# Optimization experiments

Measured on AMD Instinct MI355X. Metric: run time of the kernel, lower is better.

Reference implementation:

```python
import jax, jax.numpy as jnp
import numpy as np

B, N, S, K = 8, 4096, 2048, 64          # clouds, points/cloud, fps samples (ratio=0.5), max neighbors
C_IN, HID, OUT = 64, 128, 128
RADIUS = 0.2
EPS = 1e-5


def fps(p, s):
    """Farthest point sampling on p:[N,3]; deterministic start at index 0. Returns [s] indices."""
    def step(carry, _):
        min_d, last = carry
        d = jnp.sum((p - p[last]) ** 2, axis=-1)
        min_d = jnp.minimum(min_d, d)
        return (min_d, jnp.argmax(min_d).astype(jnp.int32)), last
    init = (jnp.full((p.shape[0],), jnp.inf, p.dtype), jnp.int32(0))
    _, idx = jax.lax.scan(step, init, None, length=s)
    return idx


def bn_act(h, g, be, mask):
    # masked batch-norm over all valid edges (training-mode stats), then ReLU
    m = mask[..., None].astype(h.dtype)
    cnt = jnp.sum(m)
    mean = jnp.sum(h * m, axis=(0, 1, 2)) / cnt
    var = jnp.sum(((h - mean) ** 2) * m, axis=(0, 1, 2)) / cnt
    return jax.nn.relu((h - mean) * jax.lax.rsqrt(var + EPS) * g + be)


def setup_inputs() -> dict:
    key = jax.random.key(0)
    ks = jax.random.split(key, 8)
    x = jax.random.normal(ks[0], (B * N, C_IN), jnp.float32)
    pos = jax.random.uniform(ks[1], (B * N, 3), jnp.float32)
    batch = jnp.repeat(jnp.arange(B, dtype=jnp.int32), N)
    c0 = C_IN + 3
    W0 = jax.random.normal(ks[2], (c0, HID), jnp.float32) / np.sqrt(c0).astype(np.float32)
    W1 = jax.random.normal(ks[3], (HID, HID), jnp.float32) / np.sqrt(HID).astype(np.float32)
    W2 = jax.random.normal(ks[4], (HID, OUT), jnp.float32) / np.sqrt(HID).astype(np.float32)
    z = lambda n: jnp.zeros((n,), jnp.float32)
    o = lambda n: jnp.ones((n,), jnp.float32)
    return dict(x=x, pos=pos, batch=batch,
                W0=W0, b0=z(HID), g0=o(HID), be0=z(HID),
                W1=W1, b1=z(HID), g1=o(HID), be1=z(HID),
                W2=W2, b2=z(OUT))


def reference(x, pos, batch, W0, b0, g0, be0, W1, b1, g1, be1, W2, b2):
    posb = pos.reshape(B, N, 3)
    xb = x.reshape(B, N, C_IN)
    idx = jax.vmap(lambda p: fps(p, S))(posb)                       # [B,S]
    ctr = jnp.take_along_axis(posb, idx[..., None], axis=1)          # [B,S,3] sampled centroids
    # radius graph: K nearest within RADIUS (mask the rest)
    d2 = jnp.sum((ctr[:, :, None, :] - posb[:, None, :, :]) ** 2, axis=-1)  # [B,S,N]
    negd, nbr = jax.lax.top_k(-d2, K)                                # [B,S,K]
    mask = (-negd) <= RADIUS ** 2
    bix = jnp.arange(B)[:, None, None]
    pos_j = posb[bix, nbr]                                           # [B,S,K,3]
    x_j = xb[bix, nbr]                                               # [B,S,K,C_IN]
    feat = jnp.concatenate([x_j, pos_j - ctr[:, :, None, :]], axis=-1)  # [B,S,K,C_IN+3]
    h = bn_act(feat @ W0 + b0, g0, be0, mask)
    h = bn_act(h @ W1 + b1, g1, be1, mask)
    h = h @ W2 + b2                                                  # plain last layer
    h = jnp.where(mask[..., None], h, -jnp.inf)
    out = jnp.max(h, axis=2)                                         # max aggregation -> [B,S,OUT]
    batch_out = jnp.take_along_axis(batch.reshape(B, N), idx, axis=1).reshape(-1)
    return out.reshape(B * S, OUT), ctr.reshape(B * S, 3), batch_out
```

## Files before the change

### kernel.cpp

```cpp
#include <hip/hip_runtime.h>

typedef _Float16 half8 __attribute__((ext_vector_type(8)));
typedef float floatx4 __attribute__((ext_vector_type(4)));

#define B_   8
#define N_   4096
#define S_   2048
#define K_   64
#define CIN  64
#define HID_ 128
#define Q_   (B_*S_)
#define NCONS 248

#define WS_STATS 0u
#define WS_CNTT  4096u
#define WS_W0T   4224u
#define WS_W1T   28800u
#define WS_W2T   61568u
#define WS_SC0   94336u
#define WS_SH0   94848u
#define WS_SC1   95360u
#define WS_SH1   95872u
#define WS_CNT   96384u
#define WS_NBR   161920u
#define WS_PROG  2259072u

__global__ __launch_bounds__(256) void k_prep(const float* __restrict__ W0,
        const float* __restrict__ W1, const float* __restrict__ W2,
        _Float16* __restrict__ w0t, _Float16* __restrict__ w1t, _Float16* __restrict__ w2t,
        unsigned long long* __restrict__ stats, int* __restrict__ cntT, int* __restrict__ prog) {
    int t = blockIdx.x * 256 + threadIdx.x;
    if (t < 128 * 96) {
        int c = t / 96, k = t - c * 96;
        w0t[t] = (k < 67) ? (_Float16)W0[k * 128 + c] : (_Float16)0.f;
    } else if (t < 128 * 96 + 16384) {
        int u = t - 128 * 96; int c = u >> 7, k = u & 127;
        w1t[u] = (_Float16)W1[k * 128 + c];
    } else if (t < 128 * 96 + 32768) {
        int u = t - 128 * 96 - 16384; int c = u >> 7, k = u & 127;
        w2t[u] = (_Float16)W2[k * 128 + c];
    }
    if (t < 512) stats[t] = 0ULL;
    if (t < 8) prog[t] = 0;
    if (t == 0) *cntT = 0;
}

template<int CTRL>
__device__ inline unsigned long long dpp64(unsigned long long v) {
    int lo = (int)(unsigned)v, hi = (int)(unsigned)(v >> 32);
    int nlo = __builtin_amdgcn_update_dpp(lo, lo, CTRL, 0xF, 0xF, false);
    int nhi = __builtin_amdgcn_update_dpp(hi, hi, CTRL, 0xF, 0xF, false);
    return ((unsigned long long)(unsigned)nhi << 32) | (unsigned long long)(unsigned)nlo;
}
__device__ inline unsigned long long u64max(unsigned long long a, unsigned long long b) {
    return (b > a) ? b : a;
}

__global__ __launch_bounds__(256) void k_front(const float* __restrict__ pos,
        const float* __restrict__ x, const _Float16* __restrict__ w0t,
        const float* __restrict__ b0, float* outCtr, float* __restrict__ outBatch,
        unsigned short* __restrict__ nbrG, int* __restrict__ cnt, int* __restrict__ cntT,
        unsigned long long* __restrict__ statsOut, int* prog) {
    __shared__ __align__(16) char uLDS[69760];
    int tid = threadIdx.x;

    if (blockIdx.x < 8) {
        float4* sP4 = (float4*)uLDS;
        unsigned long long* red = (unsigned long long*)(uLDS + 65536);
        unsigned short* sSeq = (unsigned short*)(uLDS + 65600);
        int b = blockIdx.x;
        const float* P = pos + (size_t)b * N_ * 3;

        float px[16], py[16], pz[16], md[16];
        {
            const float4* vp = (const float4*)(P + tid * 48);
            float a[48];
            #pragma unroll
            for (int v = 0; v < 12; v++) {
                float4 t4 = vp[v];
                a[v*4] = t4.x; a[v*4+1] = t4.y; a[v*4+2] = t4.z; a[v*4+3] = t4.w;
            }
            #pragma unroll
            for (int j = 0; j < 16; j++) {
                px[j] = a[3*j]; py[j] = a[3*j+1]; pz[j] = a[3*j+2];
                md[j] = __builtin_inff();
                sP4[tid * 16 + j] = make_float4(px[j], py[j], pz[j], 0.f);
            }
        }
        __syncthreads();

        int last = 0;
        for (int i = 0; i < S_; i++) {
            float4 cc = sP4[last];
            if (tid == (i & 255)) sSeq[i] = (unsigned short)last;
            unsigned long long best;
            {
                #pragma clang fp contract(off)
                float bv = -1.f; unsigned bi = 0;
                #pragma unroll
                for (int j = 0; j < 16; j++) {
                    float dx = px[j] - cc.x, dy = py[j] - cc.y, dz = pz[j] - cc.z;
                    float d = (dx * dx + dy * dy) + dz * dz;
                    float m = fminf(md[j], d); md[j] = m;
                    if (m > bv) { bv = m; bi = (unsigned)j; }
                }
                best = ((unsigned long long)__float_as_uint(bv) << 32)
                     | (unsigned long long)(0xFFFFu - (unsigned)(tid * 16) - bi);
            }
            best = u64max(best, dpp64<0x111>(best));
            best = u64max(best, dpp64<0x112>(best));
            best = u64max(best, dpp64<0x114>(best));
            best = u64max(best, dpp64<0x118>(best));
            best = u64max(best, dpp64<0x142>(best));
            best = u64max(best, dpp64<0x143>(best));
            if ((tid & 63) == 63) red[(i & 1) * 4 + (tid >> 6)] = best;
            __syncthreads();
            ulonglong2 ra = *(const ulonglong2*)&red[(i & 1) * 4];
            ulonglong2 rb = *(const ulonglong2*)&red[(i & 1) * 4 + 2];
            unsigned long long g = u64max(u64max(ra.x, ra.y), u64max(rb.x, rb.y));
            last = (int)(0xFFFFu - (unsigned)(g & 0xFFFFu));
            if ((i & 63) == 63) {
                if (tid < 64) {
                    int ii = i - 63 + tid;
                    float4 c = sP4[sSeq[ii]];
                    size_t o = (size_t)b * S_ + ii;
                    __hip_atomic_store(&outCtr[o*3],   c.x, __ATOMIC_RELAXED, __HIP_MEMORY_SCOPE_AGENT);
                    __hip_atomic_store(&outCtr[o*3+1], c.y, __ATOMIC_RELAXED, __HIP_MEMORY_SCOPE_AGENT);
                    __hip_atomic_store(&outCtr[o*3+2], c.z, __ATOMIC_RELAXED, __HIP_MEMORY_SCOPE_AGENT);
                    outBatch[o] = (float)b;
                }
                __syncthreads();
                if (tid == 0)
                    __hip_atomic_store(&prog[b], i + 1, __ATOMIC_RELEASE, __HIP_MEMORY_SCOPE_AGENT);
            }
        }
    } else {
        float* cD = (float*)uLDS;
        unsigned short* cI = (unsigned short*)(uLDS + 4096);
        unsigned short* sNbr = (unsigned short*)(uLDS + 6144);
        float* sB0v = (float*)(uLDS + 6272);
        float* sCtr = (float*)(uLDS + 6784);
        int* cN = (int*)(uLDS + 6800);
        _Float16* sBuf = (_Float16*)(uLDS + 6912);

        int wid = tid >> 6, lane = tid & 63;
        int lr = lane & 15, lq = lane >> 4;
        int colbase = 32 * wid + lr;
        half8 w0f[3][2];
        #pragma unroll
        for (int ks = 0; ks < 3; ks++)
            #pragma unroll
            for (int nt = 0; nt < 2; nt++)
                w0f[ks][nt] = *(const half8*)(w0t + (colbase + 16*nt) * 96 + ks * 32 + lq * 8);
        if (tid < 128) sB0v[tid] = b0[tid];
        float runS1[2] = {0.f, 0.f}, runS2[2] = {0.f, 0.f};

        for (int k = (int)blockIdx.x - 8; k < Q_; k += NCONS) {
            int i = k >> 3, b = k & 7;
            int q = (b << 11) + i;
            if (tid == 0) {
                while (__hip_atomic_load(&prog[b], __ATOMIC_ACQUIRE, __HIP_MEMORY_SCOPE_AGENT) <= i)
                    __builtin_amdgcn_s_sleep(32);
                sCtr[0] = __hip_atomic_load(&outCtr[(size_t)q*3],   __ATOMIC_RELAXED, __HIP_MEMORY_SCOPE_AGENT);
                sCtr[1] = __hip_atomic_load(&outCtr[(size_t)q*3+1], __ATOMIC_RELAXED, __HIP_MEMORY_SCOPE_AGENT);
                sCtr[2] = __hip_atomic_load(&outCtr[(size_t)q*3+2], __ATOMIC_RELAXED, __HIP_MEMORY_SCOPE_AGENT);
                *cN = 0;
            }
            __syncthreads();
            float cx = sCtr[0], cy = sCtr[1], cz = sCtr[2];
            const float* P = pos + (size_t)b * N_ * 3;
            float a[48];
            {
                const float4* vp = (const float4*)(P + (size_t)tid * 48);
                #pragma unroll
                for (int v = 0; v < 12; v++) {
                    float4 t4 = vp[v];
                    a[v*4] = t4.x; a[v*4+1] = t4.y; a[v*4+2] = t4.z; a[v*4+3] = t4.w;
                }
            }
            unsigned msk = 0;
            float d2a[16];
            {
                #pragma clang fp contract(off)
                #pragma unroll
                for (int j = 0; j < 16; j++) {
                    float dx = cx - a[3*j], dy = cy - a[3*j+1], dz = cz - a[3*j+2];
                    float d2 = (dx * dx + dy * dy) + dz * dz;
                    d2a[j] = d2;
                    if (d2 <= 0.04f) msk |= 1u << j;
                }
            }
            int myc = __popc(msk);
            int base = 0;
            if (myc) base = atomicAdd(cN, myc);
            unsigned mm = msk;
            while (mm) {
                int j = __builtin_ctz(mm); mm &= mm - 1;
                if (base < 1024) { cD[base] = d2a[j]; cI[base] = (unsigned short)(tid * 16 + j); }
                base++;
            }
            __syncthreads();
            int M = min(*cN, 1024);
            int n = min(M, K_);
            for (int i2 = tid; i2 < M; i2 += 256) {
                float di = cD[i2]; int ii = (int)cI[i2]; int r = 0;
                for (int j = 0; j < M; j++) {
                    float dj = cD[j];
                    r += (dj < di) || (dj == di && (int)cI[j] < ii);
                }
                if (r < K_) { nbrG[q * K_ + r] = (unsigned short)ii; sNbr[r] = (unsigned short)ii; }
            }
            if (tid == 0) { cnt[q] = n; atomicAdd(cntT, n); }
            __syncthreads();
            {
                int row = tid >> 2, c4 = (tid & 3) * 16;
                half8 o0, o1;
                #pragma unroll
                for (int e = 0; e < 8; e++) { o0[e] = (_Float16)0.f; o1[e] = (_Float16)0.f; }
                if (row < n) {
                    const float4* xr = (const float4*)(x + ((size_t)b * N_ + sNbr[row]) * CIN + c4);
                    float4 v0 = xr[0], v1 = xr[1], v2 = xr[2], v3 = xr[3];
                    o0[0]=(_Float16)v0.x; o0[1]=(_Float16)v0.y; o0[2]=(_Float16)v0.z; o0[3]=(_Float16)v0.w;
                    o0[4]=(_Float16)v1.x; o0[5]=(_Float16)v1.y; o0[6]=(_Float16)v1.z; o0[7]=(_Float16)v1.w;
                    o1[0]=(_Float16)v2.x; o1[1]=(_Float16)v2.y; o1[2]=(_Float16)v2.z; o1[3]=(_Float16)v2.w;
                    o1[4]=(_Float16)v3.x; o1[5]=(_Float16)v3.y; o1[6]=(_Float16)v3.z; o1[7]=(_Float16)v3.w;
                }
                *(half8*)&sBuf[row * 104 + c4]     = o0;
                *(half8*)&sBuf[row * 104 + c4 + 8] = o1;
            }
            if (tid < 64) {
                half8 z, o;
                #pragma unroll
                for (int e = 0; e < 8; e++) { z[e] = (_Float16)0.f; o[e] = (_Float16)0.f; }
                if (tid < n) {
                    int j = sNbr[tid];
                    const float* pj = pos + ((size_t)b * N_ + j) * 3;
                    o[0] = (_Float16)(pj[0] - cx); o[1] = (_Float16)(pj[1] - cy); o[2] = (_Float16)(pj[2] - cz);
                }
                *(half8*)&sBuf[tid * 104 + 64] = o;
                *(half8*)&sBuf[tid * 104 + 72] = z;
                *(half8*)&sBuf[tid * 104 + 80] = z;
                *(half8*)&sBuf[tid * 104 + 88] = z;
            }
            __syncthreads();
            floatx4 acc[4][2];
            #pragma unroll
            for (int rt = 0; rt < 4; rt++)
                #pragma unroll
                for (int nt = 0; nt < 2; nt++)
                    #pragma unroll
                    for (int r = 0; r < 4; r++) acc[rt][nt][r] = 0.f;
            #pragma unroll
            for (int ks = 0; ks < 3; ks++) {
                half8 av[4];
                #pragma unroll
                for (int rt = 0; rt < 4; rt++)
                    av[rt] = *(const half8*)&sBuf[(rt * 16 + lr) * 104 + ks * 32 + lq * 8];
                #pragma unroll
                for (int rt = 0; rt < 4; rt++)
                    #pragma unroll
                    for (int nt = 0; nt < 2; nt++)
                        acc[rt][nt] = __builtin_amdgcn_mfma_f32_16x16x32_f16(av[rt], w0f[ks][nt], acc[rt][nt], 0, 0, 0);
            }
            #pragma unroll
            for (int nt = 0; nt < 2; nt++) {
                int col = colbase + 16 * nt;
                float bias = sB0v[col];
                #pragma unroll
                for (int rt = 0; rt < 4; rt++) {
                    int r0 = rt * 16 + lq * 4;
                    #pragma unroll
                    for (int r = 0; r < 4; r++) {
                        float v = acc[rt][nt][r] + bias;
                        if (r0 + r < n) { runS1[nt] += v; runS2[nt] += v * v; }
                    }
                }
            }
        }
        #pragma unroll
        for (int nt = 0; nt < 2; nt++) {
            float s1 = runS1[nt], s2 = runS2[nt];
            s1 += __shfl_xor(s1, 16); s1 += __shfl_xor(s1, 32);
            s2 += __shfl_xor(s2, 16); s2 += __shfl_xor(s2, 32);
            if (lq == 0) {
                int col = colbase + 16 * nt;
                atomicAdd(&statsOut[col],       (unsigned long long)(long long)llrintf(s1 * 1048576.f));
                atomicAdd(&statsOut[128 + col], (unsigned long long)(long long)llrintf(s2 * 1048576.f));
            }
        }
    }
}

__global__ void k_bnparam(const unsigned long long* __restrict__ stats, const int* __restrict__ cntT,
        const float* __restrict__ g, const float* __restrict__ be,
        float* __restrict__ scale, float* __restrict__ shift) {
    int t = threadIdx.x;
    double c = (double)(*cntT);
    double mean = (double)(long long)stats[t] * (1.0 / 1048576.0) / c;
    double ex2  = (double)(long long)stats[128 + t] * (1.0 / 1048576.0) / c;
    double var = ex2 - mean * mean;
    if (var < 0.0) var = 0.0;
    double sc = (double)g[t] / sqrt(var + 1e-5);
    scale[t] = (float)sc;
    shift[t] = (float)((double)be[t] - mean * sc);
}

template<int STAGE>
__global__ __launch_bounds__(256, 2) void k_mlp(const float* __restrict__ x,
        const float* __restrict__ pos, const float* __restrict__ ctr,
        const unsigned short* __restrict__ nbr, const int* __restrict__ cnt,
        const _Float16* __restrict__ w0t, const _Float16* __restrict__ w1t,
        const _Float16* __restrict__ w2t,
        const float* __restrict__ b0, const float* __restrict__ b1,
        const float* __restrict__ b2,
        const float* __restrict__ sc0, const float* __restrict__ sh0,
        const float* __restrict__ sc1, const float* __restrict__ sh1,
        unsigned long long* __restrict__ statsOut, float* __restrict__ outF) {
    __shared__ __align__(16) _Float16 sBuf[64 * 136];
    __shared__ unsigned short sNbr[64];
    __shared__ float sB0v[128];
    __shared__ float sB1v[128];
    __shared__ float sSc0[128];
    __shared__ float sSh0[128];
    __shared__ float sB2v[(STAGE >= 2) ? 128 : 4];
    __shared__ float sSc1[(STAGE >= 2) ? 128 : 4];
    __shared__ float sSh1[(STAGE >= 2) ? 128 : 4];

    int tid = threadIdx.x, wid = tid >> 6, lane = tid & 63;
    int lr = lane & 15, lq = lane >> 4;
    int colbase = 32 * wid + lr;

    half8 w0f[3][2];
    #pragma unroll
    for (int ks = 0; ks < 3; ks++)
        #pragma unroll
        for (int nt = 0; nt < 2; nt++)
            w0f[ks][nt] = *(const half8*)(w0t + (colbase + 16*nt) * 96 + ks * 32 + lq * 8);
    half8 w1f[4][2];
    #pragma unroll
    for (int ks = 0; ks < 4; ks++)
        #pragma unroll
        for (int nt = 0; nt < 2; nt++)
            w1f[ks][nt] = *(const half8*)(w1t + (colbase + 16*nt) * 128 + ks * 32 + lq * 8);
    half8 w2f[(STAGE >= 2) ? 4 : 1][2];
    if constexpr (STAGE >= 2)
        #pragma unroll
        for (int ks = 0; ks < 4; ks++)
            #pragma unroll
            for (int nt = 0; nt < 2; nt++)
                w2f[ks][nt] = *(const half8*)(w2t + (colbase + 16*nt) * 128 + ks * 32 + lq * 8);

    if (tid < 128) {
        sB0v[tid] = b0[tid];
        sB1v[tid] = b1[tid]; sSc0[tid] = sc0[tid]; sSh0[tid] = sh0[tid];
        if constexpr (STAGE >= 2) { sB2v[tid] = b2[tid]; sSc1[tid] = sc1[tid]; sSh1[tid] = sh1[tid]; }
    }
    float runS1[2] = {0.f, 0.f}, runS2[2] = {0.f, 0.f};

    for (int qq = 0; qq < 8; qq++) {
        int q = blockIdx.x * 8 + qq;
        int b = q >> 11;
        __syncthreads();
        int n = cnt[q];
        if (tid < 64) sNbr[tid] = nbr[q * K_ + tid];
        __syncthreads();
        {
            int row = tid >> 2, c4 = (tid & 3) * 16;
            half8 o0, o1;
            #pragma unroll
            for (int e = 0; e < 8; e++) { o0[e] = (_Float16)0.f; o1[e] = (_Float16)0.f; }
            if (row < n) {
                const float4* xr = (const float4*)(x + ((size_t)b * N_ + sNbr[row]) * CIN + c4);
                float4 v0 = xr[0], v1 = xr[1], v2 = xr[2], v3 = xr[3];
                o0[0]=(_Float16)v0.x; o0[1]=(_Float16)v0.y; o0[2]=(_Float16)v0.z; o0[3]=(_Float16)v0.w;
                o0[4]=(_Float16)v1.x; o0[5]=(_Float16)v1.y; o0[6]=(_Float16)v1.z; o0[7]=(_Float16)v1.w;
                o1[0]=(_Float16)v2.x; o1[1]=(_Float16)v2.y; o1[2]=(_Float16)v2.z; o1[3]=(_Float16)v2.w;
                o1[4]=(_Float16)v3.x; o1[5]=(_Float16)v3.y; o1[6]=(_Float16)v3.z; o1[7]=(_Float16)v3.w;
            }
            *(half8*)&sBuf[row * 104 + c4]     = o0;
            *(half8*)&sBuf[row * 104 + c4 + 8] = o1;
        }
        if (tid < 64) {
            half8 z, o;
            #pragma unroll
            for (int e = 0; e < 8; e++) { z[e] = (_Float16)0.f; o[e] = (_Float16)0.f; }
            if (tid < n) {
                int j = sNbr[tid];
                float cx = ctr[q*3], cy = ctr[q*3+1], cz = ctr[q*3+2];
                const float* pj = pos + ((size_t)b * N_ + j) * 3;
                o[0] = (_Float16)(pj[0] - cx); o[1] = (_Float16)(pj[1] - cy); o[2] = (_Float16)(pj[2] - cz);
            }
            *(half8*)&sBuf[tid * 104 + 64] = o;
            *(half8*)&sBuf[tid * 104 + 72] = z;
            *(half8*)&sBuf[tid * 104 + 80] = z;
            *(half8*)&sBuf[tid * 104 + 88] = z;
        }
        __syncthreads();

        floatx4 acc[4][2];
        #pragma unroll
        for (int rt = 0; rt < 4; rt++)
            #pragma unroll
            for (int nt = 0; nt < 2; nt++)
                #pragma unroll
                for (int r = 0; r < 4; r++) acc[rt][nt][r] = 0.f;
        #pragma unroll
        for (int ks = 0; ks < 3; ks++) {
            half8 av[4];
            #pragma unroll
            for (int rt = 0; rt < 4; rt++)
                av[rt] = *(const half8*)&sBuf[(rt * 16 + lr) * 104 + ks * 32 + lq * 8];
            #pragma unroll
            for (int rt = 0; rt < 4; rt++)
                #pragma unroll
                for (int nt = 0; nt < 2; nt++)
                    acc[rt][nt] = __builtin_amdgcn_mfma_f32_16x16x32_f16(av[rt], w0f[ks][nt], acc[rt][nt], 0, 0, 0);
        }
        __syncthreads();

        #pragma unroll
        for (int nt = 0; nt < 2; nt++) {
            int col = colbase + 16 * nt;
            float bias = sB0v[col], s = sSc0[col], t2 = sSh0[col];
            #pragma unroll
            for (int rt = 0; rt < 4; rt++) {
                int r0 = rt * 16 + lq * 4;
                #pragma unroll
                for (int r = 0; r < 4; r++) {
                    float v = (acc[rt][nt][r] + bias) * s + t2;
                    sBuf[(r0 + r) * 136 + col] = (_Float16)fmaxf(v, 0.f);
                }
            }
        }
        __syncthreads();
        #pragma unroll
        for (int rt = 0; rt < 4; rt++)
            #pragma unroll
            for (int nt = 0; nt < 2; nt++)
                #pragma unroll
                for (int r = 0; r < 4; r++) acc[rt][nt][r] = 0.f;
        #pragma unroll
        for (int ks = 0; ks < 4; ks++) {
            half8 av[4];
            #pragma unroll
            for (int rt = 0; rt < 4; rt++)
                av[rt] = *(const half8*)&sBuf[(rt * 16 + lr) * 136 + ks * 32 + lq * 8];
            #pragma unroll
            for (int rt = 0; rt < 4; rt++)
                #pragma unroll
                for (int nt = 0; nt < 2; nt++)
                    acc[rt][nt] = __builtin_amdgcn_mfma_f32_16x16x32_f16(av[rt], w1f[ks][nt], acc[rt][nt], 0, 0, 0);
        }

        if constexpr (STAGE == 1) {
            #pragma unroll
            for (int nt = 0; nt < 2; nt++) {
                int col = colbase + 16 * nt;
                float bias = sB1v[col];
                #pragma unroll
                for (int rt = 0; rt < 4; rt++) {
                    int r0 = rt * 16 + lq * 4;
                    #pragma unroll
                    for (int r = 0; r < 4; r++) {
                        float v = acc[rt][nt][r] + bias;
                        if (r0 + r < n) { runS1[nt] += v; runS2[nt] += v * v; }
                    }
                }
            }
        } else {
            __syncthreads();
            #pragma unroll
            for (int nt = 0; nt < 2; nt++) {
                int col = colbase + 16 * nt;
                float bias = sB1v[col], s = sSc1[col], t2 = sSh1[col];
                #pragma unroll
                for (int rt = 0; rt < 4; rt++) {
                    int r0 = rt * 16 + lq * 4;
                    #pragma unroll
                    for (int r = 0; r < 4; r++) {
                        float v = (acc[rt][nt][r] + bias) * s + t2;
                        sBuf[(r0 + r) * 136 + col] = (_Float16)fmaxf(v, 0.f);
                    }
                }
            }
            __syncthreads();
            #pragma unroll
            for (int rt = 0; rt < 4; rt++)
                #pragma unroll
                for (int nt = 0; nt < 2; nt++)
                    #pragma unroll
                    for (int r = 0; r < 4; r++) acc[rt][nt][r] = 0.f;
            #pragma unroll
            for (int ks = 0; ks < 4; ks++) {
                half8 av[4];
                #pragma unroll
                for (int rt = 0; rt < 4; rt++)
                    av[rt] = *(const half8*)&sBuf[(rt * 16 + lr) * 136 + ks * 32 + lq * 8];
                #pragma unroll
                for (int rt = 0; rt < 4; rt++)
                    #pragma unroll
                    for (int nt = 0; nt < 2; nt++)
                        acc[rt][nt] = __builtin_amdgcn_mfma_f32_16x16x32_f16(av[rt], w2f[ks][nt], acc[rt][nt], 0, 0, 0);
            }
            #pragma unroll
            for (int nt = 0; nt < 2; nt++) {
                int col = colbase + 16 * nt;
                float bias = sB2v[col];
                float m = -__builtin_inff();
                #pragma unroll
                for (int rt = 0; rt < 4; rt++) {
                    int r0 = rt * 16 + lq * 4;
                    #pragma unroll
                    for (int r = 0; r < 4; r++)
                        if (r0 + r < n) m = fmaxf(m, acc[rt][nt][r] + bias);
                }
                m = fmaxf(m, __shfl_xor(m, 16));
                m = fmaxf(m, __shfl_xor(m, 32));
                if (lq == 0) outF[(size_t)q * 128 + col] = m;
            }
        }
    }
    if constexpr (STAGE == 1) {
        #pragma unroll
        for (int nt = 0; nt < 2; nt++) {
            float s1 = runS1[nt], s2 = runS2[nt];
            s1 += __shfl_xor(s1, 16); s1 += __shfl_xor(s1, 32);
            s2 += __shfl_xor(s2, 16); s2 += __shfl_xor(s2, 32);
            if (lq == 0) {
                int col = colbase + 16 * nt;
                atomicAdd(&statsOut[col],       (unsigned long long)(long long)llrintf(s1 * 1048576.f));
                atomicAdd(&statsOut[128 + col], (unsigned long long)(long long)llrintf(s2 * 1048576.f));
            }
        }
    }
}

extern "C" void kernel_launch(void* const* d_in, const int* in_sizes, int n_in,
                              void* d_out, int out_size, void* d_ws, size_t ws_size,
                              hipStream_t stream) {
    const float* x   = (const float*)d_in[0];
    const float* pos = (const float*)d_in[1];
    const float* W0  = (const float*)d_in[3];
    const float* b0  = (const float*)d_in[4];
    const float* g0  = (const float*)d_in[5];
    const float* be0 = (const float*)d_in[6];
    const float* W1  = (const float*)d_in[7];
    const float* b1  = (const float*)d_in[8];
    const float* g1  = (const float*)d_in[9];
    const float* be1 = (const float*)d_in[10];
    const float* W2  = (const float*)d_in[11];
    const float* b2  = (const float*)d_in[12];

    char* ws = (char*)d_ws;
    unsigned long long* stats = (unsigned long long*)(ws + WS_STATS);
    int* cntT = (int*)(ws + WS_CNTT);
    _Float16* w0t = (_Float16*)(ws + WS_W0T);
    _Float16* w1t = (_Float16*)(ws + WS_W1T);
    _Float16* w2t = (_Float16*)(ws + WS_W2T);
    float* sc0 = (float*)(ws + WS_SC0);
    float* sh0 = (float*)(ws + WS_SH0);
    float* sc1 = (float*)(ws + WS_SC1);
    float* sh1 = (float*)(ws + WS_SH1);
    int* cnt = (int*)(ws + WS_CNT);
    unsigned short* nbr = (unsigned short*)(ws + WS_NBR);
    int* prog = (int*)(ws + WS_PROG);

    float* outF = (float*)d_out;
    float* outCtr = (float*)d_out + 2097152;
    float* outBatch = (float*)d_out + 2146304;

    k_prep<<<176, 256, 0, stream>>>(W0, W1, W2, w0t, w1t, w2t, stats, cntT, prog);
    k_front<<<256, 256, 0, stream>>>(pos, x, w0t, b0, outCtr, outBatch, nbr, cnt, cntT,
            stats, prog);
    k_bnparam<<<1, 128, 0, stream>>>(stats, cntT, g0, be0, sc0, sh0);
    k_mlp<1><<<Q_/8, 256, 0, stream>>>(x, pos, outCtr, nbr, cnt, w0t, w1t, w2t,
            b0, b1, b2, sc0, sh0, sc1, sh1, stats + 256, outF);
    k_bnparam<<<1, 128, 0, stream>>>(stats + 256, cntT, g1, be1, sc1, sh1);
    k_mlp<2><<<Q_/8, 256, 0, stream>>>(x, pos, outCtr, nbr, cnt, w0t, w1t, w2t,
            b0, b1, b2, sc0, sh0, sc1, sh1, stats, outF);
}
```

Baseline: 1.743 ms.

## Materialize first-layer pre-activations in workspace to skip recomputation in MLP stages

```diff
diff --git a/kernel.cpp b/kernel.cpp
--- a/kernel.cpp
+++ b/kernel.cpp
@@ -24,6 +24,8 @@
 #define WS_CNT   96384u
 #define WS_NBR   161920u
 #define WS_PROG  2259072u
+#define WS_H0    2260992u
+#define H0_BYTES 268435456ULL
 
 __global__ __launch_bounds__(256) void k_prep(const float* __restrict__ W0,
         const float* __restrict__ W1, const float* __restrict__ W2,
@@ -60,8 +62,9 @@
         const float* __restrict__ x, const _Float16* __restrict__ w0t,
         const float* __restrict__ b0, float* outCtr, float* __restrict__ outBatch,
         unsigned short* __restrict__ nbrG, int* __restrict__ cnt, int* __restrict__ cntT,
-        unsigned long long* __restrict__ statsOut, int* prog) {
-    __shared__ __align__(16) char uLDS[69760];
+        unsigned long long* __restrict__ statsOut, int* prog,
+        _Float16* __restrict__ h0, int doH0) {
+    __shared__ __align__(16) char uLDS[84480];
     int tid = threadIdx.x;
 
     if (blockIdx.x < 8) {
@@ -142,6 +145,7 @@
         float* sCtr = (float*)(uLDS + 6784);
         int* cN = (int*)(uLDS + 6800);
         _Float16* sBuf = (_Float16*)(uLDS + 6912);
+        _Float16* sOut = (_Float16*)(uLDS + 20224);
 
         int wid = tid >> 6, lane = tid & 63;
         int lr = lane & 15, lq = lane >> 4;
@@ -273,8 +277,15 @@
                     for (int r = 0; r < 4; r++) {
                         float v = acc[rt][nt][r] + bias;
                         if (r0 + r < n) { runS1[nt] += v; runS2[nt] += v * v; }
+                        if (doH0) sOut[(r0 + r) * 128 + col] = (_Float16)v;
                     }
                 }
+            }
+            if (doH0) {
+                __syncthreads();
+                const float4* src = (const float4*)sOut;
+                float4* dst = (float4*)(h0 + (size_t)q * 8192);
+                for (int i2 = tid; i2 < 1024; i2 += 256) dst[i2] = src[i2];
             }
         }
         #pragma unroll
@@ -305,7 +316,7 @@
     shift[t] = (float)((double)be[t] - mean * sc);
 }
 
-template<int STAGE>
+template<int STAGE, int BIG>
 __global__ __launch_bounds__(256, 2) void k_mlp(const float* __restrict__ x,
         const float* __restrict__ pos, const float* __restrict__ ctr,
         const unsigned short* __restrict__ nbr, const int* __restrict__ cnt,
@@ -315,7 +326,8 @@
         const float* __restrict__ b2,
         const float* __restrict__ sc0, const float* __restrict__ sh0,
         const float* __restrict__ sc1, const float* __restrict__ sh1,
-        unsigned long long* __restrict__ statsOut, float* __restrict__ outF) {
+        unsigned long long* __restrict__ statsOut, const _Float16* __restrict__ h0,
+        float* __restrict__ outF) {
     __shared__ __align__(16) _Float16 sBuf[64 * 136];
     __shared__ unsigned short sNbr[64];
     __shared__ float sB0v[128];
@@ -330,12 +342,13 @@
     int lr = lane & 15, lq = lane >> 4;
     int colbase = 32 * wid + lr;
 
-    half8 w0f[3][2];
-    #pragma unroll
-    for (int ks = 0; ks < 3; ks++)
-        #pragma unroll
-        for (int nt = 0; nt < 2; nt++)
-            w0f[ks][nt] = *(const half8*)(w0t + (colbase + 16*nt) * 96 + ks * 32 + lq * 8);
+    half8 w0f[BIG ? 1 : 3][2];
+    if constexpr (!BIG)
+        #pragma unroll
+        for (int ks = 0; ks < 3; ks++)
+            #pragma unroll
+            for (int nt = 0; nt < 2; nt++)
+                w0f[ks][nt] = *(const half8*)(w0t + (colbase + 16*nt) * 96 + ks * 32 + lq * 8);
     half8 w1f[4][2];
     #pragma unroll
     for (int ks = 0; ks < 4; ks++)
@@ -362,77 +375,95 @@
         int b = q >> 11;
         __syncthreads();
         int n = cnt[q];
-        if (tid < 64) sNbr[tid] = nbr[q * K_ + tid];
-        __syncthreads();
-        {
-            int row = tid >> 2, c4 = (tid & 3) * 16;
-            half8 o0, o1;
-            #pragma unroll
-            for (int e = 0; e < 8; e++) { o0[e] = (_Float16)0.f; o1[e] = (_Float16)0.f; }
-            if (row < n) {
-                const float4* xr = (const float4*)(x + ((size_t)b * N_ + sNbr[row]) * CIN + c4);
-                float4 v0 = xr[0], v1 = xr[1], v2 = xr[2], v3 = xr[3];
-                o0[0]=(_Float16)v0.x; o0[1]=(_Float16)v0.y; o0[2]=(_Float16)v0.z; o0[3]=(_Float16)v0.w;
-                o0[4]=(_Float16)v1.x; o0[5]=(_Float16)v1.y; o0[6]=(_Float16)v1.z; o0[7]=(_Float16)v1.w;
-                o1[0]=(_Float16)v2.x; o1[1]=(_Float16)v2.y; o1[2]=(_Float16)v2.z; o1[3]=(_Float16)v2.w;
-                o1[4]=(_Float16)v3.x; o1[5]=(_Float16)v3.y; o1[6]=(_Float16)v3.z; o1[7]=(_Float16)v3.w;
-            }
-            *(half8*)&sBuf[row * 104 + c4]     = o0;
-            *(half8*)&sBuf[row * 104 + c4 + 8] = o1;
-        }
-        if (tid < 64) {
-            half8 z, o;
-            #pragma unroll
-            for (int e = 0; e < 8; e++) { z[e] = (_Float16)0.f; o[e] = (_Float16)0.f; }
-            if (tid < n) {
-                int j = sNbr[tid];
-                float cx = ctr[q*3], cy = ctr[q*3+1], cz = ctr[q*3+2];
-                const float* pj = pos + ((size_t)b * N_ + j) * 3;
-                o[0] = (_Float16)(pj[0] - cx); o[1] = (_Float16)(pj[1] - cy); o[2] = (_Float16)(pj[2] - cz);
-            }
-            *(half8*)&sBuf[tid * 104 + 64] = o;
-            *(half8*)&sBuf[tid * 104 + 72] = z;
-            *(half8*)&sBuf[tid * 104 + 80] = z;
-            *(half8*)&sBuf[tid * 104 + 88] = z;
-        }
-        __syncthreads();
-
         floatx4 acc[4][2];
-        #pragma unroll
-        for (int rt = 0; rt < 4; rt++)
-            #pragma unroll
-            for (int nt = 0; nt < 2; nt++)
-                #pragma unroll
-                for (int r = 0; r < 4; r++) acc[rt][nt][r] = 0.f;
-        #pragma unroll
-        for (int ks = 0; ks < 3; ks++) {
-            half8 av[4];
+
+        if constexpr (BIG) {
+            int row = tid >> 2, c0 = (tid & 3) * 32;
+            const _Float16* hp = h0 + (size_t)q * 8192 + row * 128 + c0;
+            #pragma unroll
+            for (int g2 = 0; g2 < 4; g2++) {
+                half8 hv = *(const half8*)(hp + g2 * 8);
+                half8 ov;
+                #pragma unroll
+                for (int e = 0; e < 8; e++) {
+                    int c = c0 + g2 * 8 + e;
+                    float v = (float)hv[e] * sSc0[c] + sSh0[c];
+                    ov[e] = (_Float16)fmaxf(v, 0.f);
+                }
+                *(half8*)&sBuf[row * 136 + c0 + g2 * 8] = ov;
+            }
+            __syncthreads();
+        } else {
+            if (tid < 64) sNbr[tid] = nbr[q * K_ + tid];
+            __syncthreads();
+            {
+                int row = tid >> 2, c4 = (tid & 3) * 16;
+                half8 o0, o1;
+                #pragma unroll
+                for (int e = 0; e < 8; e++) { o0[e] = (_Float16)0.f; o1[e] = (_Float16)0.f; }
+                if (row < n) {
+                    const float4* xr = (const float4*)(x + ((size_t)b * N_ + sNbr[row]) * CIN + c4);
+                    float4 v0 = xr[0], v1 = xr[1], v2 = xr[2], v3 = xr[3];
+                    o0[0]=(_Float16)v0.x; o0[1]=(_Float16)v0.y; o0[2]=(_Float16)v0.z; o0[3]=(_Float16)v0.w;
+                    o0[4]=(_Float16)v1.x; o0[5]=(_Float16)v1.y; o0[6]=(_Float16)v1.z; o0[7]=(_Float16)v1.w;
+                    o1[0]=(_Float16)v2.x; o1[1]=(_Float16)v2.y; o1[2]=(_Float16)v2.z; o1[3]=(_Float16)v2.w;
+                    o1[4]=(_Float16)v3.x; o1[5]=(_Float16)v3.y; o1[6]=(_Float16)v3.z; o1[7]=(_Float16)v3.w;
+                }
+                *(half8*)&sBuf[row * 104 + c4]     = o0;
+                *(half8*)&sBuf[row * 104 + c4 + 8] = o1;
+            }
+            if (tid < 64) {
+                half8 z, o;
+                #pragma unroll
+                for (int e = 0; e < 8; e++) { z[e] = (_Float16)0.f; o[e] = (_Float16)0.f; }
+                if (tid < n) {
+                    int j = sNbr[tid];
+                    float cx = ctr[q*3], cy = ctr[q*3+1], cz = ctr[q*3+2];
+                    const float* pj = pos + ((size_t)b * N_ + j) * 3;
+                    o[0] = (_Float16)(pj[0] - cx); o[1] = (_Float16)(pj[1] - cy); o[2] = (_Float16)(pj[2] - cz);
+                }
+                *(half8*)&sBuf[tid * 104 + 64] = o;
+                *(half8*)&sBuf[tid * 104 + 72] = z;
+                *(half8*)&sBuf[tid * 104 + 80] = z;
+                *(half8*)&sBuf[tid * 104 + 88] = z;
+            }
+            __syncthreads();
             #pragma unroll
             for (int rt = 0; rt < 4; rt++)
-                av[rt] = *(const half8*)&sBuf[(rt * 16 + lr) * 104 + ks * 32 + lq * 8];
-            #pragma unroll
-            for (int rt = 0; rt < 4; rt++)
                 #pragma unroll
                 for (int nt = 0; nt < 2; nt++)
-                    acc[rt][nt] = __builtin_amdgcn_mfma_f32_16x16x32_f16(av[rt], w0f[ks][nt], acc[rt][nt], 0, 0, 0);
-        }
-        __syncthreads();
-
-        #pragma unroll
-        for (int nt = 0; nt < 2; nt++) {
-            int col = colbase + 16 * nt;
-            float bias = sB0v[col], s = sSc0[col], t2 = sSh0[col];
-            #pragma unroll
-            for (int rt = 0; rt < 4; rt++) {
-                int r0 = rt * 16 + lq * 4;
-                #pragma unroll
-                for (int r = 0; r < 4; r++) {
-                    float v = (acc[rt][nt][r] + bias) * s + t2;
-                    sBuf[(r0 + r) * 136 + col] = (_Float16)fmaxf(v, 0.f);
-                }
-            }
-        }
-        __syncthreads();
+                    #pragma unroll
+                    for (int r = 0; r < 4; r++) acc[rt][nt][r] = 0.f;
+            #pragma unroll
+            for (int ks = 0; ks < 3; ks++) {
+                half8 av[4];
+                #pragma unroll
+                for (int rt = 0; rt < 4; rt++)
+                    av[rt] = *(const half8*)&sBuf[(rt * 16 + lr) * 104 + ks * 32 + lq * 8];
+                #pragma unroll
+                for (int rt = 0; rt < 4; rt++)
+                    #pragma unroll
+                    for (int nt = 0; nt < 2; nt++)
+                        acc[rt][nt] = __builtin_amdgcn_mfma_f32_16x16x32_f16(av[rt], w0f[ks][nt], acc[rt][nt], 0, 0, 0);
+            }
+            __syncthreads();
+            #pragma unroll
+            for (int nt = 0; nt < 2; nt++) {
+                int col = colbase + 16 * nt;
+                float bias = sB0v[col], s = sSc0[col], t2 = sSh0[col];
+                #pragma unroll
+                for (int rt = 0; rt < 4; rt++) {
+                    int r0 = rt * 16 + lq * 4;
+                    #pragma unroll
+                    for (int r = 0; r < 4; r++) {
+                        float v = (acc[rt][nt][r] + bias) * s + t2;
+                        sBuf[(r0 + r) * 136 + col] = (_Float16)fmaxf(v, 0.f);
+                    }
+                }
+            }
+            __syncthreads();
+        }
+
         #pragma unroll
         for (int rt = 0; rt < 4; rt++)
             #pragma unroll
@@ -564,6 +595,8 @@
     int* cnt = (int*)(ws + WS_CNT);
     unsigned short* nbr = (unsigned short*)(ws + WS_NBR);
     int* prog = (int*)(ws + WS_PROG);
+    _Float16* h0 = (_Float16*)(ws + WS_H0);
+    int big = (ws_size >= (size_t)WS_H0 + H0_BYTES) ? 1 : 0;
 
     float* outF = (float*)d_out;
     float* outCtr = (float*)d_out + 2097152;
@@ -571,11 +604,19 @@
 
     k_prep<<<176, 256, 0, stream>>>(W0, W1, W2, w0t, w1t, w2t, stats, cntT, prog);
     k_front<<<256, 256, 0, stream>>>(pos, x, w0t, b0, outCtr, outBatch, nbr, cnt, cntT,
-            stats, prog);
+            stats, prog, h0, big);
     k_bnparam<<<1, 128, 0, stream>>>(stats, cntT, g0, be0, sc0, sh0);
-    k_mlp<1><<<Q_/8, 256, 0, stream>>>(x, pos, outCtr, nbr, cnt, w0t, w1t, w2t,
-            b0, b1, b2, sc0, sh0, sc1, sh1, stats + 256, outF);
-    k_bnparam<<<1, 128, 0, stream>>>(stats + 256, cntT, g1, be1, sc1, sh1);
-    k_mlp<2><<<Q_/8, 256, 0, stream>>>(x, pos, outCtr, nbr, cnt, w0t, w1t, w2t,
-            b0, b1, b2, sc0, sh0, sc1, sh1, stats, outF);
+    if (big) {
+        k_mlp<1,1><<<Q_/8, 256, 0, stream>>>(x, pos, outCtr, nbr, cnt, w0t, w1t, w2t,
+                b0, b1, b2, sc0, sh0, sc1, sh1, stats + 256, h0, outF);
+        k_bnparam<<<1, 128, 0, stream>>>(stats + 256, cntT, g1, be1, sc1, sh1);
+        k_mlp<2,1><<<Q_/8, 256, 0, stream>>>(x, pos, outCtr, nbr, cnt, w0t, w1t, w2t,
+                b0, b1, b2, sc0, sh0, sc1, sh1, stats, h0, outF);
+    } else {
+        k_mlp<1,0><<<Q_/8, 256, 0, stream>>>(x, pos, outCtr, nbr, cnt, w0t, w1t, w2t,
+                b0, b1, b2, sc0, sh0, sc1, sh1, stats + 256, h0, outF);
+        k_bnparam<<<1, 128, 0, stream>>>(stats + 256, cntT, g1, be1, sc1, sh1);
+        k_mlp<2,0><<<Q_/8, 256, 0, stream>>>(x, pos, outCtr, nbr, cnt, w0t, w1t, w2t,
+                b0, b1, b2, sc0, sh0, sc1, sh1, stats, h0, outF);
+    }
 }
```

Result: no change. 1.749 ms (+0.4%).

## Fold BN param kernels into MLP, publish FPS indices instead of centroids

Applied to the files above, without the earlier changes.

```diff
diff --git a/kernel.cpp b/kernel.cpp
--- a/kernel.cpp
+++ b/kernel.cpp
@@ -17,13 +17,10 @@
 #define WS_W0T   4224u
 #define WS_W1T   28800u
 #define WS_W2T   61568u
-#define WS_SC0   94336u
-#define WS_SH0   94848u
-#define WS_SC1   95360u
-#define WS_SH1   95872u
 #define WS_CNT   96384u
 #define WS_NBR   161920u
 #define WS_PROG  2259072u
+#define WS_IDX   2259200u
 
 __global__ __launch_bounds__(256) void k_prep(const float* __restrict__ W0,
         const float* __restrict__ W1, const float* __restrict__ W2,
@@ -58,10 +55,10 @@
 
 __global__ __launch_bounds__(256) void k_front(const float* __restrict__ pos,
         const float* __restrict__ x, const _Float16* __restrict__ w0t,
-        const float* __restrict__ b0, float* outCtr, float* __restrict__ outBatch,
+        const float* __restrict__ b0, float* __restrict__ outCtr, float* __restrict__ outBatch,
         unsigned short* __restrict__ nbrG, int* __restrict__ cnt, int* __restrict__ cntT,
-        unsigned long long* __restrict__ statsOut, int* prog) {
-    __shared__ __align__(16) char uLDS[69760];
+        unsigned long long* __restrict__ statsOut, int* prog, int* idxG) {
+    __shared__ __align__(16) char uLDS[84480];
     int tid = threadIdx.x;
 
     if (blockIdx.x < 8) {
@@ -122,17 +119,20 @@
             if ((i & 63) == 63) {
                 if (tid < 64) {
                     int ii = i - 63 + tid;
-                    float4 c = sP4[sSeq[ii]];
-                    size_t o = (size_t)b * S_ + ii;
-                    __hip_atomic_store(&outCtr[o*3],   c.x, __ATOMIC_RELAXED, __HIP_MEMORY_SCOPE_AGENT);
-                    __hip_atomic_store(&outCtr[o*3+1], c.y, __ATOMIC_RELAXED, __HIP_MEMORY_SCOPE_AGENT);
-                    __hip_atomic_store(&outCtr[o*3+2], c.z, __ATOMIC_RELAXED, __HIP_MEMORY_SCOPE_AGENT);
-                    outBatch[o] = (float)b;
+                    __hip_atomic_store(&idxG[b * S_ + ii], (int)sSeq[ii],
+                                       __ATOMIC_RELAXED, __HIP_MEMORY_SCOPE_AGENT);
                 }
                 __syncthreads();
                 if (tid == 0)
                     __hip_atomic_store(&prog[b], i + 1, __ATOMIC_RELEASE, __HIP_MEMORY_SCOPE_AGENT);
             }
+        }
+        __syncthreads();
+        for (int i = tid; i < S_; i += 256) {
+            int o = b * S_ + i;
+            float4 c = sP4[sSeq[i]];
+            outCtr[o*3] = c.x; outCtr[o*3+1] = c.y; outCtr[o*3+2] = c.z;
+            outBatch[o] = (float)b;
         }
     } else {
         float* cD = (float*)uLDS;
@@ -161,9 +161,9 @@
             if (tid == 0) {
                 while (__hip_atomic_load(&prog[b], __ATOMIC_ACQUIRE, __HIP_MEMORY_SCOPE_AGENT) <= i)
                     __builtin_amdgcn_s_sleep(32);
-                sCtr[0] = __hip_atomic_load(&outCtr[(size_t)q*3],   __ATOMIC_RELAXED, __HIP_MEMORY_SCOPE_AGENT);
-                sCtr[1] = __hip_atomic_load(&outCtr[(size_t)q*3+1], __ATOMIC_RELAXED, __HIP_MEMORY_SCOPE_AGENT);
-                sCtr[2] = __hip_atomic_load(&outCtr[(size_t)q*3+2], __ATOMIC_RELAXED, __HIP_MEMORY_SCOPE_AGENT);
+                int idx = __hip_atomic_load(&idxG[b * S_ + i], __ATOMIC_RELAXED, __HIP_MEMORY_SCOPE_AGENT);
+                const float* pc = pos + ((size_t)b * N_ + idx) * 3;
+                sCtr[0] = pc[0]; sCtr[1] = pc[1]; sCtr[2] = pc[2];
                 *cN = 0;
             }
             __syncthreads();
@@ -291,30 +291,19 @@
     }
 }
 
-__global__ void k_bnparam(const unsigned long long* __restrict__ stats, const int* __restrict__ cntT,
-        const float* __restrict__ g, const float* __restrict__ be,
-        float* __restrict__ scale, float* __restrict__ shift) {
-    int t = threadIdx.x;
-    double c = (double)(*cntT);
-    double mean = (double)(long long)stats[t] * (1.0 / 1048576.0) / c;
-    double ex2  = (double)(long long)stats[128 + t] * (1.0 / 1048576.0) / c;
-    double var = ex2 - mean * mean;
-    if (var < 0.0) var = 0.0;
-    double sc = (double)g[t] / sqrt(var + 1e-5);
-    scale[t] = (float)sc;
-    shift[t] = (float)((double)be[t] - mean * sc);
-}
-
 template<int STAGE>
-__global__ __launch_bounds__(256, 2) void k_mlp(const float* __restrict__ x,
+__global__ __launch_bounds__(256, 3) void k_mlp(const float* __restrict__ x,
         const float* __restrict__ pos, const float* __restrict__ ctr,
         const unsigned short* __restrict__ nbr, const int* __restrict__ cnt,
         const _Float16* __restrict__ w0t, const _Float16* __restrict__ w1t,
         const _Float16* __restrict__ w2t,
         const float* __restrict__ b0, const float* __restrict__ b1,
         const float* __restrict__ b2,
-        const float* __restrict__ sc0, const float* __restrict__ sh0,
-        const float* __restrict__ sc1, const float* __restrict__ sh1,
+        const float* __restrict__ g0, const float* __restrict__ be0,
+        const float* __restrict__ g1, const float* __restrict__ be1,
+        const int* __restrict__ cntT,
+        const unsigned long long* __restrict__ stats0,
+        const unsigned long long* __restrict__ stats1,
         unsigned long long* __restrict__ statsOut, float* __restrict__ outF) {
     __shared__ __align__(16) _Float16 sBuf[64 * 136];
     __shared__ unsigned short sNbr[64];
@@ -330,6 +319,29 @@
     int lr = lane & 15, lq = lane >> 4;
     int colbase = 32 * wid + lr;
 
+    if (tid < 128) {
+        double c = (double)(*cntT);
+        double mean = (double)(long long)stats0[tid] * (1.0 / 1048576.0) / c;
+        double ex2  = (double)(long long)stats0[128 + tid] * (1.0 / 1048576.0) / c;
+        double var = ex2 - mean * mean;
+        if (var < 0.0) var = 0.0;
+        double sc = (double)g0[tid] / sqrt(var + 1e-5);
+        sSc0[tid] = (float)sc;
+        sSh0[tid] = (float)((double)be0[tid] - mean * sc);
+        sB0v[tid] = b0[tid];
+        sB1v[tid] = b1[tid];
+        if constexpr (STAGE >= 2) {
+            double mean1 = (double)(long long)stats1[tid] * (1.0 / 1048576.0) / c;
+            double ex21  = (double)(long long)stats1[128 + tid] * (1.0 / 1048576.0) / c;
+            double var1 = ex21 - mean1 * mean1;
+            if (var1 < 0.0) var1 = 0.0;
+            double sc1 = (double)g1[tid] / sqrt(var1 + 1e-5);
+            sSc1[tid] = (float)sc1;
+            sSh1[tid] = (float)((double)be1[tid] - mean1 * sc1);
+            sB2v[tid] = b2[tid];
+        }
+    }
+
     half8 w0f[3][2];
     #pragma unroll
     for (int ks = 0; ks < 3; ks++)
@@ -350,11 +362,6 @@
             for (int nt = 0; nt < 2; nt++)
                 w2f[ks][nt] = *(const half8*)(w2t + (colbase + 16*nt) * 128 + ks * 32 + lq * 8);
 
-    if (tid < 128) {
-        sB0v[tid] = b0[tid];
-        sB1v[tid] = b1[tid]; sSc0[tid] = sc0[tid]; sSh0[tid] = sh0[tid];
-        if constexpr (STAGE >= 2) { sB2v[tid] = b2[tid]; sSc1[tid] = sc1[tid]; sSh1[tid] = sh1[tid]; }
-    }
     float runS1[2] = {0.f, 0.f}, runS2[2] = {0.f, 0.f};
 
     for (int qq = 0; qq < 8; qq++) {
@@ -417,7 +424,6 @@
                     acc[rt][nt] = __builtin_amdgcn_mfma_f32_16x16x32_f16(av[rt], w0f[ks][nt], acc[rt][nt], 0, 0, 0);
         }
         __syncthreads();
-
         #pragma unroll
         for (int nt = 0; nt < 2; nt++) {
             int col = colbase + 16 * nt;
@@ -557,13 +563,10 @@
     _Float16* w0t = (_Float16*)(ws + WS_W0T);
     _Float16* w1t = (_Float16*)(ws + WS_W1T);
     _Float16* w2t = (_Float16*)(ws + WS_W2T);
-    float* sc0 = (float*)(ws + WS_SC0);
-    float* sh0 = (float*)(ws + WS_SH0);
-    float* sc1 = (float*)(ws + WS_SC1);
-    float* sh1 = (float*)(ws + WS_SH1);
     int* cnt = (int*)(ws + WS_CNT);
     unsigned short* nbr = (unsigned short*)(ws + WS_NBR);
     int* prog = (int*)(ws + WS_PROG);
+    int* idxG = (int*)(ws + WS_IDX);
 
     float* outF = (float*)d_out;
     float* outCtr = (float*)d_out + 2097152;
@@ -571,11 +574,9 @@
 
     k_prep<<<176, 256, 0, stream>>>(W0, W1, W2, w0t, w1t, w2t, stats, cntT, prog);
     k_front<<<256, 256, 0, stream>>>(pos, x, w0t, b0, outCtr, outBatch, nbr, cnt, cntT,
-            stats, prog);
-    k_bnparam<<<1, 128, 0, stream>>>(stats, cntT, g0, be0, sc0, sh0);
+            stats, prog, idxG);
     k_mlp<1><<<Q_/8, 256, 0, stream>>>(x, pos, outCtr, nbr, cnt, w0t, w1t, w2t,
-            b0, b1, b2, sc0, sh0, sc1, sh1, stats + 256, outF);
-    k_bnparam<<<1, 128, 0, stream>>>(stats + 256, cntT, g1, be1, sc1, sh1);
+            b0, b1, b2, g0, be0, g1, be1, cntT, stats, stats + 256, stats + 256, outF);
     k_mlp<2><<<Q_/8, 256, 0, stream>>>(x, pos, outCtr, nbr, cnt, w0t, w1t, w2t,
-            b0, b1, b2, sc0, sh0, sc1, sh1, stats, outF);
+            b0, b1, b2, g0, be0, g1, be1, cntT, stats, stats + 256, stats, outF);
 }
```

Result: no change. 1.744 ms (+0.1%).
